# Optimization experiments

Hardware: AMD Instinct MI355X
Metric: run time of the kernel (lower is better)

## Reference

```python
import jax, jax.numpy as jnp
import numpy as np

N_NODES = 100000


def _spmm(rows, cols, vals, x):
    # out[i] = sum over edges e with rows[e]==i of vals[e] * x[cols[e]]
    gathered = x[cols] * vals[:, None]          # [E, F]
    return jax.ops.segment_sum(gathered, rows, num_segments=N_NODES)


def setup_inputs() -> dict:
    key = jax.random.key(0)
    ks = jax.random.split(key, 8)
    E = 3200000
    features = jax.random.normal(ks[0], (N_NODES, 128), dtype=jnp.float32)
    adj_rows = jnp.sort(jax.random.randint(ks[1], (E,), 0, N_NODES))
    adj_cols = jax.random.randint(ks[2], (E,), 0, N_NODES)
    adj_vals = jax.random.uniform(ks[3], (E,), dtype=jnp.float32)
    W1 = jax.random.normal(ks[4], (128, 128), dtype=jnp.float32) * 0.05
    b1 = jnp.zeros((128,), dtype=jnp.float32)
    W2 = jax.random.normal(ks[5], (128, 128), dtype=jnp.float32) * 0.05
    b2 = jnp.zeros((128,), dtype=jnp.float32)
    return {"features": features, "adj_rows": adj_rows, "adj_cols": adj_cols,
            "adj_vals": adj_vals, "W1": W1, "b1": b1, "W2": W2, "b2": b2}


def reference(features, adj_rows, adj_cols, adj_vals, W1, b1, W2, b2):
    # GC layer 1: adj @ (x @ W1) + b1
    h = _spmm(adj_rows, adj_cols, adj_vals, features @ W1) + b1
    h = jax.nn.relu(h)
    # GC layer 2: adj @ (h @ W2) + b2
    out = _spmm(adj_rows, adj_cols, adj_vals, h @ W2) + b2
    return out
```

## Files before the change

kernel.cpp:

```cpp
#include <hip/hip_runtime.h>
#include <type_traits>

#define FDIM 128

typedef __attribute__((ext_vector_type(8))) short short8v;
typedef __attribute__((ext_vector_type(4))) float f32x4;

__device__ __forceinline__ uint16_t f2bf(float f) {
    uint32_t u = __float_as_uint(f);
    uint32_t r = (u + 0x7fffu + ((u >> 16) & 1u)) >> 16;
    return (uint16_t)r;
}
__device__ __forceinline__ uint32_t pack_bf16(float a, float b) {
    return (uint32_t)f2bf(a) | ((uint32_t)f2bf(b) << 16);
}
__device__ __forceinline__ float bflo(uint32_t u) { return __uint_as_float(u << 16); }
__device__ __forceinline__ float bfhi(uint32_t u) { return __uint_as_float(u & 0xffff0000u); }

__global__ __launch_bounds__(256) void build_row_ptr_k(const int* __restrict__ rows,
                                                       int E, int N,
                                                       int* __restrict__ rp) {
    int i = blockIdx.x * 256 + threadIdx.x;
    if (i > N) return;
    int lo = 0, hi = E;
    while (lo < hi) {
        int mid = (lo + hi) >> 1;
        if (rows[mid] < i) lo = mid + 1; else hi = mid;
    }
    rp[i] = lo;
}

__global__ __launch_bounds__(256) void transpose_w_k(const float* __restrict__ W,
                                                     uint16_t* __restrict__ Wt) {
    int idx = blockIdx.x * 256 + threadIdx.x;
    int k = idx >> 7, n = idx & 127;
    Wt[n * FDIM + k] = f2bf(W[k * FDIM + n]);
}

template <int ABF>
__global__ __launch_bounds__(256) void gemm_mfma_k(const void* __restrict__ A_,
                                                   const uint16_t* __restrict__ Wt,
                                                   uint16_t* __restrict__ C, int M) {
    const int t = threadIdx.x;
    const int w = t >> 6;
    const int l = t & 63;
    const int row0 = blockIdx.x * 128 + w * 32;

    f32x4 acc[2][8];
#pragma unroll
    for (int mf = 0; mf < 2; ++mf)
#pragma unroll
        for (int nf = 0; nf < 8; ++nf) acc[mf][nf] = (f32x4)0.f;

    const int lr = l & 15;
    const int kg = l >> 4;

#pragma unroll
    for (int ks = 0; ks < 4; ++ks) {
        const int k0 = ks * 32 + kg * 8;
        short8v a[2];
#pragma unroll
        for (int mf = 0; mf < 2; ++mf) {
            int r = row0 + mf * 16 + lr;
            if (r >= M) r = M - 1;
            if constexpr (ABF) {
                a[mf] = *(const short8v*)((const uint16_t*)A_ + (size_t)r * FDIM + k0);
            } else {
                const float* ap = (const float*)A_ + (size_t)r * FDIM + k0;
                float4 f0 = *(const float4*)(ap);
                float4 f1 = *(const float4*)(ap + 4);
                uint32_t p0 = pack_bf16(f0.x, f0.y), p1 = pack_bf16(f0.z, f0.w);
                uint32_t p2 = pack_bf16(f1.x, f1.y), p3 = pack_bf16(f1.z, f1.w);
                uint4 u = make_uint4(p0, p1, p2, p3);
                a[mf] = *(short8v*)&u;
            }
        }
#pragma unroll
        for (int nf = 0; nf < 8; ++nf) {
            short8v b = *(const short8v*)(Wt + (size_t)(nf * 16 + lr) * FDIM + k0);
            acc[0][nf] = __builtin_amdgcn_mfma_f32_16x16x32_bf16(a[0], b, acc[0][nf], 0, 0, 0);
            acc[1][nf] = __builtin_amdgcn_mfma_f32_16x16x32_bf16(a[1], b, acc[1][nf], 0, 0, 0);
        }
    }

    const int colpar = l & 1;
#pragma unroll
    for (int mf = 0; mf < 2; ++mf) {
#pragma unroll
        for (int nf = 0; nf < 8; ++nf) {
            int col = nf * 16 + lr;
#pragma unroll
            for (int j = 0; j < 4; ++j) {
                float v = acc[mf][nf][j];
                float pv = __shfl_xor(v, 1);
                int row = row0 + mf * 16 + kg * 4 + j;
                if (!colpar && row < M) {
                    *(uint32_t*)(C + (size_t)row * FDIM + col) = pack_bf16(v, pv);
                }
            }
        }
    }
}

template <int RELU, int OBF>
__global__ __launch_bounds__(256) void spmm_k(const int* __restrict__ rp,
                                              const int* __restrict__ cols,
                                              const float* __restrict__ vals,
                                              const uint32_t* __restrict__ X,
                                              const float* __restrict__ bias,
                                              void* __restrict__ out, int N) {
    int wid  = (blockIdx.x * 256 + threadIdx.x) >> 6;
    int lane = threadIdx.x & 63;
    if (wid >= N) return;
    int s = __builtin_amdgcn_readfirstlane(rp[wid]);
    int e = __builtin_amdgcn_readfirstlane(rp[wid + 1]);

    float ax[8], ay[8];
#pragma unroll
    for (int j = 0; j < 8; ++j) { ax[j] = 0.f; ay[j] = 0.f; }

    const int nfull = (e - s) >> 3;
    int i = s;
    int cc[8];

    if (nfull > 0) {
#pragma unroll
        for (int j = 0; j < 8; ++j) cc[j] = __builtin_amdgcn_readfirstlane(cols[i + j]);
        for (int g = 1; g < nfull; ++g) {
            int cn[8];
#pragma unroll
            for (int j = 0; j < 8; ++j) cn[j] = __builtin_amdgcn_readfirstlane(cols[i + 8 + j]);
            uint32_t u[8];
#pragma unroll
            for (int j = 0; j < 8; ++j) u[j] = X[(size_t)cc[j] * 64 + lane];
#pragma unroll
            for (int j = 0; j < 8; ++j) {
                float v = vals[i + j];
                ax[j] = fmaf(v, bflo(u[j]), ax[j]);
                ay[j] = fmaf(v, bfhi(u[j]), ay[j]);
            }
#pragma unroll
            for (int j = 0; j < 8; ++j) cc[j] = cn[j];
            i += 8;
        }
        {
            uint32_t u[8];
#pragma unroll
            for (int j = 0; j < 8; ++j) u[j] = X[(size_t)cc[j] * 64 + lane];
#pragma unroll
            for (int j = 0; j < 8; ++j) {
                float v = vals[i + j];
                ax[j] = fmaf(v, bflo(u[j]), ax[j]);
                ay[j] = fmaf(v, bfhi(u[j]), ay[j]);
            }
            i += 8;
        }
    }
    for (; i < e; ++i) {
        int c = __builtin_amdgcn_readfirstlane(cols[i]);
        float v = vals[i];
        uint32_t u = X[(size_t)c * 64 + lane];
        ax[0] = fmaf(v, bflo(u), ax[0]);
        ay[0] = fmaf(v, bfhi(u), ay[0]);
    }

    float ox = ((ax[0] + ax[1]) + (ax[2] + ax[3])) + ((ax[4] + ax[5]) + (ax[6] + ax[7]));
    float oy = ((ay[0] + ay[1]) + (ay[2] + ay[3])) + ((ay[4] + ay[5]) + (ay[6] + ay[7]));
    ox += bias[lane * 2];
    oy += bias[lane * 2 + 1];
    if (RELU) { ox = fmaxf(ox, 0.f); oy = fmaxf(oy, 0.f); }

    if constexpr (OBF) {
        ((uint32_t*)out)[(size_t)wid * 64 + lane] = pack_bf16(ox, oy);
    } else {
        *(float2*)((float*)out + (size_t)wid * FDIM + lane * 2) = make_float2(ox, oy);
    }
}

extern "C" void kernel_launch(void* const* d_in, const int* in_sizes, int n_in,
                              void* d_out, int out_size, void* d_ws, size_t ws_size,
                              hipStream_t stream) {
    const float* features = (const float*)d_in[0];
    const int*   adj_rows = (const int*)d_in[1];
    const int*   adj_cols = (const int*)d_in[2];
    const float* adj_vals = (const float*)d_in[3];
    const float* W1       = (const float*)d_in[4];
    const float* b1       = (const float*)d_in[5];
    const float* W2       = (const float*)d_in[6];
    const float* b2       = (const float*)d_in[7];

    const int N = in_sizes[0] / FDIM;
    const int E = in_sizes[1];
    float* out = (float*)d_out;

    char* ws = (char*)d_ws;
    int* rp = (int*)ws;
    size_t rp_bytes = (((size_t)(N + 1) * sizeof(int)) + 255) & ~(size_t)255;
    uint16_t* XWb = (uint16_t*)(ws + rp_bytes);
    uint16_t* Hb  = XWb + (size_t)N * FDIM;
    uint16_t* W1t = Hb + (size_t)N * FDIM;
    uint16_t* W2t = W1t + FDIM * FDIM;

    const int nblk = (N + 127) / 128;

    build_row_ptr_k<<<(N + 256) / 256, 256, 0, stream>>>(adj_rows, E, N, rp);
    transpose_w_k<<<64, 256, 0, stream>>>(W1, W1t);
    transpose_w_k<<<64, 256, 0, stream>>>(W2, W2t);
    gemm_mfma_k<0><<<nblk, 256, 0, stream>>>((const void*)features, W1t, XWb, N);
    spmm_k<1, 1><<<((size_t)N * 64 + 255) / 256, 256, 0, stream>>>(
        rp, adj_cols, adj_vals, (const uint32_t*)XWb, b1, (void*)Hb, N);
    gemm_mfma_k<1><<<nblk, 256, 0, stream>>>((const void*)Hb, W2t, XWb, N);
    spmm_k<0, 0><<<((size_t)N * 64 + 255) / 256, 256, 0, stream>>>(
        rp, adj_cols, adj_vals, (const uint32_t*)XWb, b2, (void*)out, N);
}
```

Before: 291.0 us.

## Slice feature matrix into column blocks for cache-resident SpMM gathers

```diff
diff --git a/kernel.cpp b/kernel.cpp
--- a/kernel.cpp
+++ b/kernel.cpp
@@ -2,6 +2,7 @@
 #include <type_traits>
 
 #define FDIM 128
+#define NSLICE 8
 
 typedef __attribute__((ext_vector_type(8))) short short8v;
 typedef __attribute__((ext_vector_type(4))) float f32x4;
@@ -16,6 +17,7 @@
 }
 __device__ __forceinline__ float bflo(uint32_t u) { return __uint_as_float(u << 16); }
 __device__ __forceinline__ float bfhi(uint32_t u) { return __uint_as_float(u & 0xffff0000u); }
+
 
 __global__ __launch_bounds__(256) void build_row_ptr_k(const int* __restrict__ rows,
                                                        int E, int N,
@@ -40,7 +42,7 @@
 template <int ABF>
 __global__ __launch_bounds__(256) void gemm_mfma_k(const void* __restrict__ A_,
                                                    const uint16_t* __restrict__ Wt,
-                                                   uint16_t* __restrict__ C, int M) {
+                                                   uint32_t* __restrict__ C, int M) {
     const int t = threadIdx.x;
     const int w = t >> 6;
     const int l = t & 63;
@@ -64,7 +66,9 @@
             int r = row0 + mf * 16 + lr;
             if (r >= M) r = M - 1;
             if constexpr (ABF) {
-                a[mf] = *(const short8v*)((const uint16_t*)A_ + (size_t)r * FDIM + k0);
+                const uint16_t* ap = (const uint16_t*)A_ +
+                    (size_t)(k0 >> 4) * ((size_t)M * 16) + (size_t)r * 16 + (k0 & 15);
+                a[mf] = *(const short8v*)ap;
             } else {
                 const float* ap = (const float*)A_ + (size_t)r * FDIM + k0;
                 float4 f0 = *(const float4*)(ap);
@@ -88,92 +92,78 @@
     for (int mf = 0; mf < 2; ++mf) {
 #pragma unroll
         for (int nf = 0; nf < 8; ++nf) {
-            int col = nf * 16 + lr;
 #pragma unroll
             for (int j = 0; j < 4; ++j) {
                 float v = acc[mf][nf][j];
                 float pv = __shfl_xor(v, 1);
                 int row = row0 + mf * 16 + kg * 4 + j;
                 if (!colpar && row < M) {
-                    *(uint32_t*)(C + (size_t)row * FDIM + col) = pack_bf16(v, pv);
+                    C[(size_t)nf * ((size_t)M * 8) + (size_t)row * 8 + (lr >> 1)] =
+                        pack_bf16(v, pv);
                 }
             }
         }
     }
 }
 
-template <int RELU, int OBF>
-__global__ __launch_bounds__(256) void spmm_k(const int* __restrict__ rp,
-                                              const int* __restrict__ cols,
-                                              const float* __restrict__ vals,
-                                              const uint32_t* __restrict__ X,
-                                              const float* __restrict__ bias,
-                                              void* __restrict__ out, int N) {
-    int wid  = (blockIdx.x * 256 + threadIdx.x) >> 6;
-    int lane = threadIdx.x & 63;
-    if (wid >= N) return;
-    int s = __builtin_amdgcn_readfirstlane(rp[wid]);
-    int e = __builtin_amdgcn_readfirstlane(rp[wid + 1]);
-
-    float ax[8], ay[8];
-#pragma unroll
-    for (int j = 0; j < 8; ++j) { ax[j] = 0.f; ay[j] = 0.f; }
-
-    const int nfull = (e - s) >> 3;
-    int i = s;
-    int cc[8];
-
-    if (nfull > 0) {
-#pragma unroll
-        for (int j = 0; j < 8; ++j) cc[j] = __builtin_amdgcn_readfirstlane(cols[i + j]);
-        for (int g = 1; g < nfull; ++g) {
-            int cn[8];
-#pragma unroll
-            for (int j = 0; j < 8; ++j) cn[j] = __builtin_amdgcn_readfirstlane(cols[i + 8 + j]);
-            uint32_t u[8];
-#pragma unroll
-            for (int j = 0; j < 8; ++j) u[j] = X[(size_t)cc[j] * 64 + lane];
-#pragma unroll
-            for (int j = 0; j < 8; ++j) {
-                float v = vals[i + j];
-                ax[j] = fmaf(v, bflo(u[j]), ax[j]);
-                ay[j] = fmaf(v, bfhi(u[j]), ay[j]);
-            }
-#pragma unroll
-            for (int j = 0; j < 8; ++j) cc[j] = cn[j];
-            i += 8;
-        }
-        {
-            uint32_t u[8];
-#pragma unroll
-            for (int j = 0; j < 8; ++j) u[j] = X[(size_t)cc[j] * 64 + lane];
-#pragma unroll
-            for (int j = 0; j < 8; ++j) {
-                float v = vals[i + j];
-                ax[j] = fmaf(v, bflo(u[j]), ax[j]);
-                ay[j] = fmaf(v, bfhi(u[j]), ay[j]);
-            }
-            i += 8;
-        }
-    }
-    for (; i < e; ++i) {
-        int c = __builtin_amdgcn_readfirstlane(cols[i]);
-        float v = vals[i];
-        uint32_t u = X[(size_t)c * 64 + lane];
-        ax[0] = fmaf(v, bflo(u), ax[0]);
-        ay[0] = fmaf(v, bfhi(u), ay[0]);
-    }
-
-    float ox = ((ax[0] + ax[1]) + (ax[2] + ax[3])) + ((ax[4] + ax[5]) + (ax[6] + ax[7]));
-    float oy = ((ay[0] + ay[1]) + (ay[2] + ay[3])) + ((ay[4] + ay[5]) + (ay[6] + ay[7]));
-    ox += bias[lane * 2];
-    oy += bias[lane * 2 + 1];
-    if (RELU) { ox = fmaxf(ox, 0.f); oy = fmaxf(oy, 0.f); }
-
-    if constexpr (OBF) {
-        ((uint32_t*)out)[(size_t)wid * 64 + lane] = pack_bf16(ox, oy);
-    } else {
-        *(float2*)((float*)out + (size_t)wid * FDIM + lane * 2) = make_float2(ox, oy);
+template <int RELU, int OUT_SLICED>
+__global__ __launch_bounds__(256) void spmm_sliced_k(const int* __restrict__ rp,
+                                                     const int* __restrict__ cols,
+                                                     const float* __restrict__ vals,
+                                                     const uint32_t* __restrict__ Xs,
+                                                     const float* __restrict__ bias,
+                                                     void* __restrict__ out, int N) {
+    const int s    = blockIdx.x & 7;
+    const int g0   = blockIdx.x >> 3;
+    const int gs   = gridDim.x >> 3;
+    const int wave = threadIdx.x >> 6;
+    const int lane = threadIdx.x & 63;
+    const int f    = lane & 7;
+    const int ep   = lane >> 3;
+    const int l31  = lane & 31;
+
+    const uint32_t* X_s = Xs + (size_t)s * ((size_t)N * 8);
+    const float2 bb = *(const float2*)(bias + s * 16 + 2 * f);
+
+    for (int r = g0 * 4 + wave; r < N; r += gs * 4) {
+        int s_ = __builtin_amdgcn_readfirstlane(rp[r]);
+        int e_ = __builtin_amdgcn_readfirstlane(rp[r + 1]);
+
+        float alo = 0.f, ahi = 0.f;
+        for (int i = s_; i < e_; i += 32) {
+            int   li = i + l31;
+            int   cl = li < e_ ? li : e_ - 1;
+            int   creg = cols[cl];
+            float vreg = (li < e_) ? vals[cl] : 0.f;
+#pragma unroll
+            for (int t = 0; t < 4; ++t) {
+                if (i + t * 8 < e_) {
+                    int   j = t * 8 + ep;
+                    int   c = __shfl(creg, j);
+                    float v = __shfl(vreg, j);
+                    uint32_t u = X_s[(size_t)c * 8 + f];
+                    alo = fmaf(v, bflo(u), alo);
+                    ahi = fmaf(v, bfhi(u), ahi);
+                }
+            }
+        }
+#pragma unroll
+        for (int m = 8; m < 64; m <<= 1) {
+            alo += __shfl_xor(alo, m);
+            ahi += __shfl_xor(ahi, m);
+        }
+        alo += bb.x; ahi += bb.y;
+        if (RELU) { alo = fmaxf(alo, 0.f); ahi = fmaxf(ahi, 0.f); }
+
+        if (ep == 0) {
+            if constexpr (OUT_SLICED) {
+                ((uint32_t*)out)[(size_t)s * ((size_t)N * 8) + (size_t)r * 8 + f] =
+                    pack_bf16(alo, ahi);
+            } else {
+                *(float2*)((float*)out + (size_t)r * FDIM + s * 16 + 2 * f) =
+                    make_float2(alo, ahi);
+            }
+        }
     }
 }
 
@@ -196,20 +186,21 @@
     char* ws = (char*)d_ws;
     int* rp = (int*)ws;
     size_t rp_bytes = (((size_t)(N + 1) * sizeof(int)) + 255) & ~(size_t)255;
-    uint16_t* XWb = (uint16_t*)(ws + rp_bytes);
-    uint16_t* Hb  = XWb + (size_t)N * FDIM;
-    uint16_t* W1t = Hb + (size_t)N * FDIM;
+    uint32_t* XWb = (uint32_t*)(ws + rp_bytes);
+    uint32_t* Hb  = XWb + (size_t)N * 64;
+    uint16_t* W1t = (uint16_t*)(Hb + (size_t)N * 64);
     uint16_t* W2t = W1t + FDIM * FDIM;
 
-    const int nblk = (N + 127) / 128;
+    const int nblk_gemm = (N + 127) / 128;
+    const int nblk_spmm = 8 * 2048;
 
     build_row_ptr_k<<<(N + 256) / 256, 256, 0, stream>>>(adj_rows, E, N, rp);
     transpose_w_k<<<64, 256, 0, stream>>>(W1, W1t);
     transpose_w_k<<<64, 256, 0, stream>>>(W2, W2t);
-    gemm_mfma_k<0><<<nblk, 256, 0, stream>>>((const void*)features, W1t, XWb, N);
-    spmm_k<1, 1><<<((size_t)N * 64 + 255) / 256, 256, 0, stream>>>(
-        rp, adj_cols, adj_vals, (const uint32_t*)XWb, b1, (void*)Hb, N);
-    gemm_mfma_k<1><<<nblk, 256, 0, stream>>>((const void*)Hb, W2t, XWb, N);
-    spmm_k<0, 0><<<((size_t)N * 64 + 255) / 256, 256, 0, stream>>>(
-        rp, adj_cols, adj_vals, (const uint32_t*)XWb, b2, (void*)out, N);
-}
+    gemm_mfma_k<0><<<nblk_gemm, 256, 0, stream>>>((const void*)features, W1t, XWb, N);
+    spmm_sliced_k<1, 1><<<nblk_spmm, 256, 0, stream>>>(rp, adj_cols, adj_vals,
+                                                       XWb, b1, (void*)Hb, N);
+    gemm_mfma_k<1><<<nblk_gemm, 256, 0, stream>>>((const void*)Hb, W2t, XWb, N);
+    spmm_sliced_k<0, 0><<<nblk_spmm, 256, 0, stream>>>(rp, adj_cols, adj_vals,
+                                                       XWb, b2, (void*)out, N);
+}
```

After: 571.0 us. 96.2% more time.
